# Performance work log

Measured on AMD Instinct MI355X. Metric: run time of the kernel, lower is better.

The kernel has to match this reference:

```python
import jax, jax.numpy as jnp
import numpy as np

IN_FEATURES = 512
DIM_EXPLOSION = 20
OUT_FEATURES = IN_FEATURES * DIM_EXPLOSION  # 10240
NB_PROJ_ENTRIES = 6
HASH_LENGTH = 32
BATCH = 4096


def _make_sparse_proj(key):
    """Sparse binary random projection: each of the OUT_FEATURES rows has
    NB_PROJ_ENTRIES entries set to 1 (as in OlfactoryModel.create_rand_proj_matrix)."""
    idx = jax.random.randint(key, (OUT_FEATURES, NB_PROJ_ENTRIES), 0, IN_FEATURES)
    rows = jnp.arange(OUT_FEATURES)[:, None]
    W = jnp.zeros((OUT_FEATURES, IN_FEATURES), dtype=jnp.float32)
    return W.at[rows, idx].set(1.0)


def setup_inputs() -> dict:
    key = jax.random.key(0)
    k1, k2 = jax.random.split(key)
    inp = jax.random.uniform(k1, (BATCH, IN_FEATURES), dtype=jnp.float32)
    W = _make_sparse_proj(k2)
    return {"input": inp, "weight": W, "hash_length": HASH_LENGTH}


def reference(input, weight, hash_length):
    # F.linear: [B, in] @ [out, in]^T -> [B, out]
    x = jnp.einsum('bi,oi->bo', input, weight)
    # MB_sparsify: winner-take-all, keep top `hash_length` activations per row, zero the rest
    topv = jax.lax.top_k(x, hash_length)[0]          # [B, k]
    thresh = topv[:, -1:]                            # k-th largest per row
    return jnp.where(x >= thresh, x, jnp.zeros_like(x))
```

## Files before the change

### kernel.cpp

```cpp
#include <hip/hip_runtime.h>


typedef float f4 __attribute__((ext_vector_type(4)));

constexpr int IN_F   = 512;
constexpr int OUT_F  = 10240;
constexpr int TPB    = 512;
constexpr int ROWS   = 4;
constexpr int FPT    = OUT_F / TPB;
constexpr int NBINS  = 1024;
constexpr int NWAVES = TPB / 64;
constexpr int CAP    = 64;

static_assert(NBINS == 64 * 16, "wave scan assumes 16 bins per lane");
static_assert(TPB == IN_F, "staging assumes one f4 per thread");

__global__ __launch_bounds__(256) void extract_idx(const float* __restrict__ W,
                                                   uint4* __restrict__ packed,
                                                   int out_f) {
  int row  = blockIdx.x * 4 + (threadIdx.x >> 6);
  int lane = threadIdx.x & 63;
  if (row >= out_f) return;

  const float* wr = W + (size_t)row * IN_F;
  unsigned long long masks[8];
#pragma unroll
  for (int c = 0; c < 8; ++c) {
    float v = wr[c * 64 + lane];
    masks[c] = __ballot(v != 0.0f);
  }
  if (lane == 0) {
    unsigned idx[6] = {IN_F, IN_F, IN_F, IN_F, IN_F, IN_F};
    int n = 0;
#pragma unroll
    for (int c = 0; c < 8; ++c) {
      unsigned long long m = masks[c];
      while (m && n < 6) {
        int b = __builtin_ctzll(m);
        idx[n++] = (unsigned)(c * 64 + b);
        m &= m - 1;
      }
    }
    uint4 r;
    r.x = idx[0] | (idx[1] << 16);
    r.y = idx[2] | (idx[3] << 16);
    r.z = idx[4] | (idx[5] << 16);
    r.w = (unsigned)n;
    packed[row] = r;
  }
}

__device__ __forceinline__ float row_val(const f4* in4, uint4 p, int r) {
  const float* b = (const float*)in4;
  float s = b[(p.x & 0xFFFFu) * 4 + r];
  s += b[(p.x >> 16) * 4 + r];
  s += b[(p.y & 0xFFFFu) * 4 + r];
  s += b[(p.y >> 16) * 4 + r];
  s += b[(p.z & 0xFFFFu) * 4 + r];
  s += b[(p.z >> 16) * 4 + r];
  return s;
}

__global__ __launch_bounds__(TPB, 4) void fly_hash(const float* __restrict__ inp,
                                                   const uint4* __restrict__ packed,
                                                   const int* __restrict__ kptr,
                                                   float* __restrict__ out) {
  __shared__ f4    in4[IN_F + 1];
  __shared__ int   hist[ROWS * NBINS];
  __shared__ int   wsum[NWAVES];
  __shared__ int   sh_bstar[ROWS], sh_above[ROWS], sh_n[ROWS], sh_cnt[ROWS];
  __shared__ float sh_list[ROWS][CAP];
  __shared__ float sh_thr[ROWS];
  __shared__ int   sh_need[ROWS];

  const int tid  = threadIdx.x;
  const int lane = tid & 63;
  const int wid  = tid >> 6;
  const int row0 = blockIdx.x * ROWS;
  const int k    = *kptr;

  {
    const float* p = inp + (size_t)row0 * IN_F + tid;
    f4 v;
    v.x = p[0];
    v.y = p[IN_F];
    v.z = p[2 * IN_F];
    v.w = p[3 * IN_F];
    in4[tid] = v;
  }
  if (tid == 0) {
    f4 z = {0.0f, 0.0f, 0.0f, 0.0f};
    in4[IN_F] = z;
  }
  if (tid < ROWS) { sh_bstar[tid] = -1; sh_cnt[tid] = 0; }
  for (int i = tid; i < ROWS * NBINS; i += TPB) hist[i] = 0;
  __syncthreads();

  f4 x4[FPT];
#pragma unroll
  for (int i = 0; i < FPT; ++i) {
    uint4 r = packed[tid + i * TPB];
    f4 s = in4[r.x & 0xFFFFu];
    s += in4[r.x >> 16];
    s += in4[r.y & 0xFFFFu];
    s += in4[r.y >> 16];
    s += in4[r.z & 0xFFFFu];
    s += in4[r.z >> 16];
    x4[i] = s;
#pragma unroll
    for (int rr = 0; rr < ROWS; ++rr) {
      float v = s[rr];
      if (v >= 4.0f) {
        int b = (int)((v - 4.0f) * 512.0f);
        b = b > NBINS - 1 ? NBINS - 1 : b;
        atomicAdd(&hist[rr * NBINS + b], 1);
      }
    }
  }
  __syncthreads();

  if (wid < ROWS) {
    const int r = wid;
    const int base = r * NBINS + lane * 16;
    int csum = 0;
#pragma unroll
    for (int j = 0; j < 16; ++j) csum += hist[base + j];
    int s = csum;
#pragma unroll
    for (int off = 1; off < 64; off <<= 1) {
      int t = __shfl_down(s, off);
      if (lane + off < 64) s += t;
    }
    int s_next = __shfl_down(s, 1);
    if (lane == 63) s_next = 0;
    if (s >= k && s_next < k) {
      int acc = s_next;
      int bsel = lane * 16, abv = s_next;
      for (int b = lane * 16 + 15; b >= lane * 16; --b) {
        int h = hist[r * NBINS + b];
        if (acc + h >= k) { bsel = b; abv = acc; break; }
        acc += h;
      }
      sh_bstar[r] = bsel;
      sh_above[r] = abv;
      sh_n[r]     = hist[r * NBINS + bsel];
    }
  }
  __syncthreads();

  {
    const int b0 = sh_bstar[0], b1 = sh_bstar[1];
    const int b2 = sh_bstar[2], b3 = sh_bstar[3];
#pragma unroll
    for (int i = 0; i < FPT; ++i) {
      f4 s = x4[i];
#pragma unroll
      for (int rr = 0; rr < ROWS; ++rr) {
        float v = s[rr];
        int bb = (rr == 0) ? b0 : (rr == 1) ? b1 : (rr == 2) ? b2 : b3;
        if (v >= 4.0f) {
          int b = (int)((v - 4.0f) * 512.0f);
          b = b > NBINS - 1 ? NBINS - 1 : b;
          if (b == bb) {
            int p = atomicAdd(&sh_cnt[rr], 1);
            if (p < CAP) sh_list[rr][p] = v;
          }
        }
      }
    }
  }
  __syncthreads();

  if (wid < ROWS) {
    const int r   = wid;
    const int bst = sh_bstar[r];
    const int n   = (bst >= 0) ? sh_n[r] : CAP + 1;
    if (bst >= 0 && n <= CAP && sh_cnt[r] <= CAP) {
      const int j = k - sh_above[r];
      float vl = (lane < n) ? sh_list[r][lane] : -1.0f;
      int cgt = 0, cge = 0;
      for (int m = 0; m < n; ++m) {
        float u = sh_list[r][m];
        cgt += (u > vl);
        cge += (u >= vl);
      }
      if (lane < n && cgt < j && cge >= j) sh_thr[r] = vl;
      if (lane == 0) sh_need[r] = 0;
    } else {
      if (lane == 0) sh_need[r] = 1;
    }
  }
  __syncthreads();

#pragma unroll 1
  for (int r = 0; r < ROWS; ++r) {
    if (!sh_need[r]) continue;
    unsigned lo = 0u, hi = __float_as_uint(8.0f);
    while (lo < hi) {
      unsigned mid = lo + ((hi - lo + 1u) >> 1);
      float fm = __uint_as_float(mid);
      int c = 0;
      for (int i = 0; i < FPT; ++i) {
        uint4 p = packed[tid + i * TPB];
        c += (int)__popcll(__ballot(row_val(in4, p, r) >= fm));
      }
      if (lane == 0) wsum[wid] = c;
      __syncthreads();
      int tot = 0;
#pragma unroll
      for (int w = 0; w < NWAVES; ++w) tot += wsum[w];
      if (tot >= k) lo = mid; else hi = mid - 1u;
      __syncthreads();
    }
    if (tid == 0) sh_thr[r] = __uint_as_float(lo);
    __syncthreads();
  }
  const float t0 = sh_thr[0];
  const float t1 = sh_thr[1];
  const float t2 = sh_thr[2];
  const float t3 = sh_thr[3];

  float* o0 = out + (size_t)(row0 + 0) * OUT_F;
  float* o1 = out + (size_t)(row0 + 1) * OUT_F;
  float* o2 = out + (size_t)(row0 + 2) * OUT_F;
  float* o3 = out + (size_t)(row0 + 3) * OUT_F;
#pragma unroll
  for (int i = 0; i < FPT; ++i) {
    int f = tid + i * TPB;
    f4 v = x4[i];
    __builtin_nontemporal_store((v.x >= t0) ? v.x : 0.0f, &o0[f]);
    __builtin_nontemporal_store((v.y >= t1) ? v.y : 0.0f, &o1[f]);
    __builtin_nontemporal_store((v.z >= t2) ? v.z : 0.0f, &o2[f]);
    __builtin_nontemporal_store((v.w >= t3) ? v.w : 0.0f, &o3[f]);
  }
}

extern "C" void kernel_launch(void* const* d_in, const int* in_sizes, int n_in,
                              void* d_out, int out_size, void* d_ws, size_t ws_size,
                              hipStream_t stream) {
  const float* inp = (const float*)d_in[0];
  const float* W   = (const float*)d_in[1];
  const int* kptr  = (const int*)d_in[2];
  float* out       = (float*)d_out;

  const int batch = in_sizes[0] / IN_F;
  const int out_f = in_sizes[1] / IN_F;

  uint4* packed = (uint4*)d_ws;

  hipLaunchKernelGGL(extract_idx, dim3((out_f + 3) / 4), dim3(256), 0, stream,
                     W, packed, out_f);
  hipLaunchKernelGGL(fly_hash, dim3(batch / ROWS), dim3(TPB), 0, stream,
                     inp, packed, kptr, out);
}
```

Baseline: 243.0 us.

## Process eight batch rows per block to reuse gathered projection indices

The block grows to 1024 threads and handles eight input rows instead of four. The rows are staged into two shared f4 arrays, so each thread's load of packed projection indices now feeds eight row sums. This halves the global index traffic per output and doubles the per-block histogram and selection state. In exchange, barriers span more waves, shared memory per block grows, and the grid has half as many blocks, which may change occupancy and tail behaviour.

After: 256.3 us. +5.5%, slower.

```diff
diff --git a/kernel.cpp b/kernel.cpp
--- a/kernel.cpp
+++ b/kernel.cpp
@@ -5,15 +5,14 @@
 
 constexpr int IN_F   = 512;
 constexpr int OUT_F  = 10240;
-constexpr int TPB    = 512;
-constexpr int ROWS   = 4;
+constexpr int TPB    = 1024;
+constexpr int ROWS   = 8;
 constexpr int FPT    = OUT_F / TPB;
 constexpr int NBINS  = 1024;
 constexpr int NWAVES = TPB / 64;
 constexpr int CAP    = 64;
 
 static_assert(NBINS == 64 * 16, "wave scan assumes 16 bins per lane");
-static_assert(TPB == IN_F, "staging assumes one f4 per thread");
 
 __global__ __launch_bounds__(256) void extract_idx(const float* __restrict__ W,
                                                    uint4* __restrict__ packed,
@@ -65,7 +64,8 @@
                                                    const uint4* __restrict__ packed,
                                                    const int* __restrict__ kptr,
                                                    float* __restrict__ out) {
-  __shared__ f4    in4[IN_F + 1];
+  __shared__ f4    in4a[IN_F + 1];
+  __shared__ f4    in4b[IN_F + 1];
   __shared__ int   hist[ROWS * NBINS];
   __shared__ int   wsum[NWAVES];
   __shared__ int   sh_bstar[ROWS], sh_above[ROWS], sh_n[ROWS], sh_cnt[ROWS];
@@ -80,40 +80,61 @@
   const int k    = *kptr;
 
   {
-    const float* p = inp + (size_t)row0 * IN_F + tid;
+    const int t = tid & 511;
+    const float* p = inp + (size_t)(row0 + (tid >> 9) * 4) * IN_F + t;
     f4 v;
     v.x = p[0];
     v.y = p[IN_F];
     v.z = p[2 * IN_F];
     v.w = p[3 * IN_F];
-    in4[tid] = v;
+    if (tid < 512) in4a[t] = v; else in4b[t] = v;
   }
   if (tid == 0) {
     f4 z = {0.0f, 0.0f, 0.0f, 0.0f};
-    in4[IN_F] = z;
+    in4a[IN_F] = z;
+    in4b[IN_F] = z;
   }
   if (tid < ROWS) { sh_bstar[tid] = -1; sh_cnt[tid] = 0; }
   for (int i = tid; i < ROWS * NBINS; i += TPB) hist[i] = 0;
   __syncthreads();
 
-  f4 x4[FPT];
+  f4 xa[FPT], xb[FPT];
 #pragma unroll
   for (int i = 0; i < FPT; ++i) {
     uint4 r = packed[tid + i * TPB];
-    f4 s = in4[r.x & 0xFFFFu];
-    s += in4[r.x >> 16];
-    s += in4[r.y & 0xFFFFu];
-    s += in4[r.y >> 16];
-    s += in4[r.z & 0xFFFFu];
-    s += in4[r.z >> 16];
-    x4[i] = s;
-#pragma unroll
-    for (int rr = 0; rr < ROWS; ++rr) {
-      float v = s[rr];
+    const unsigned i0 = r.x & 0xFFFFu, i1 = r.x >> 16;
+    const unsigned i2 = r.y & 0xFFFFu, i3 = r.y >> 16;
+    const unsigned i4 = r.z & 0xFFFFu, i5 = r.z >> 16;
+    f4 sa = in4a[i0];
+    sa += in4a[i1];
+    sa += in4a[i2];
+    sa += in4a[i3];
+    sa += in4a[i4];
+    sa += in4a[i5];
+    f4 sb = in4b[i0];
+    sb += in4b[i1];
+    sb += in4b[i2];
+    sb += in4b[i3];
+    sb += in4b[i4];
+    sb += in4b[i5];
+    xa[i] = sa;
+    xb[i] = sb;
+#pragma unroll
+    for (int rr = 0; rr < 4; ++rr) {
+      float v = sa[rr];
       if (v >= 4.0f) {
         int b = (int)((v - 4.0f) * 512.0f);
         b = b > NBINS - 1 ? NBINS - 1 : b;
         atomicAdd(&hist[rr * NBINS + b], 1);
+      }
+    }
+#pragma unroll
+    for (int rr = 0; rr < 4; ++rr) {
+      float v = sb[rr];
+      if (v >= 4.0f) {
+        int b = (int)((v - 4.0f) * 512.0f);
+        b = b > NBINS - 1 ? NBINS - 1 : b;
+        atomicAdd(&hist[(rr + 4) * NBINS + b], 1);
       }
     }
   }
@@ -151,12 +172,14 @@
   {
     const int b0 = sh_bstar[0], b1 = sh_bstar[1];
     const int b2 = sh_bstar[2], b3 = sh_bstar[3];
+    const int b4 = sh_bstar[4], b5 = sh_bstar[5];
+    const int b6 = sh_bstar[6], b7 = sh_bstar[7];
 #pragma unroll
     for (int i = 0; i < FPT; ++i) {
-      f4 s = x4[i];
-#pragma unroll
-      for (int rr = 0; rr < ROWS; ++rr) {
-        float v = s[rr];
+      f4 sa = xa[i];
+#pragma unroll
+      for (int rr = 0; rr < 4; ++rr) {
+        float v = sa[rr];
         int bb = (rr == 0) ? b0 : (rr == 1) ? b1 : (rr == 2) ? b2 : b3;
         if (v >= 4.0f) {
           int b = (int)((v - 4.0f) * 512.0f);
@@ -164,6 +187,20 @@
           if (b == bb) {
             int p = atomicAdd(&sh_cnt[rr], 1);
             if (p < CAP) sh_list[rr][p] = v;
+          }
+        }
+      }
+      f4 sb = xb[i];
+#pragma unroll
+      for (int rr = 0; rr < 4; ++rr) {
+        float v = sb[rr];
+        int bb = (rr == 0) ? b4 : (rr == 1) ? b5 : (rr == 2) ? b6 : b7;
+        if (v >= 4.0f) {
+          int b = (int)((v - 4.0f) * 512.0f);
+          b = b > NBINS - 1 ? NBINS - 1 : b;
+          if (b == bb) {
+            int p = atomicAdd(&sh_cnt[rr + 4], 1);
+            if (p < CAP) sh_list[rr + 4][p] = v;
           }
         }
       }
@@ -195,6 +232,8 @@
 #pragma unroll 1
   for (int r = 0; r < ROWS; ++r) {
     if (!sh_need[r]) continue;
+    const f4* inx = (r < 4) ? in4a : in4b;
+    const int rc  = r & 3;
     unsigned lo = 0u, hi = __float_as_uint(8.0f);
     while (lo < hi) {
       unsigned mid = lo + ((hi - lo + 1u) >> 1);
@@ -202,7 +241,7 @@
       int c = 0;
       for (int i = 0; i < FPT; ++i) {
         uint4 p = packed[tid + i * TPB];
-        c += (int)__popcll(__ballot(row_val(in4, p, r) >= fm));
+        c += (int)__popcll(__ballot(row_val(inx, p, rc) >= fm));
       }
       if (lane == 0) wsum[wid] = c;
       __syncthreads();
@@ -219,19 +258,32 @@
   const float t1 = sh_thr[1];
   const float t2 = sh_thr[2];
   const float t3 = sh_thr[3];
+  const float t4 = sh_thr[4];
+  const float t5 = sh_thr[5];
+  const float t6 = sh_thr[6];
+  const float t7 = sh_thr[7];
 
   float* o0 = out + (size_t)(row0 + 0) * OUT_F;
   float* o1 = out + (size_t)(row0 + 1) * OUT_F;
   float* o2 = out + (size_t)(row0 + 2) * OUT_F;
   float* o3 = out + (size_t)(row0 + 3) * OUT_F;
+  float* o4 = out + (size_t)(row0 + 4) * OUT_F;
+  float* o5 = out + (size_t)(row0 + 5) * OUT_F;
+  float* o6 = out + (size_t)(row0 + 6) * OUT_F;
+  float* o7 = out + (size_t)(row0 + 7) * OUT_F;
 #pragma unroll
   for (int i = 0; i < FPT; ++i) {
     int f = tid + i * TPB;
-    f4 v = x4[i];
-    __builtin_nontemporal_store((v.x >= t0) ? v.x : 0.0f, &o0[f]);
-    __builtin_nontemporal_store((v.y >= t1) ? v.y : 0.0f, &o1[f]);
-    __builtin_nontemporal_store((v.z >= t2) ? v.z : 0.0f, &o2[f]);
-    __builtin_nontemporal_store((v.w >= t3) ? v.w : 0.0f, &o3[f]);
+    f4 va = xa[i];
+    f4 vb = xb[i];
+    __builtin_nontemporal_store((va.x >= t0) ? va.x : 0.0f, &o0[f]);
+    __builtin_nontemporal_store((va.y >= t1) ? va.y : 0.0f, &o1[f]);
+    __builtin_nontemporal_store((va.z >= t2) ? va.z : 0.0f, &o2[f]);
+    __builtin_nontemporal_store((va.w >= t3) ? va.w : 0.0f, &o3[f]);
+    __builtin_nontemporal_store((vb.x >= t4) ? vb.x : 0.0f, &o4[f]);
+    __builtin_nontemporal_store((vb.y >= t5) ? vb.y : 0.0f, &o5[f]);
+    __builtin_nontemporal_store((vb.z >= t6) ? vb.z : 0.0f, &o6[f]);
+    __builtin_nontemporal_store((vb.w >= t7) ? vb.w : 0.0f, &o7[f]);
   }
 }
 
```
